# Optimization experiments

Measured on AMD Instinct MI355X. Metric: run time of the kernel, lower is better.

## Reference

```python
import jax, jax.numpy as jnp
import numpy as np

N, E = 50000, 1_000_000
IN_F, OUT_F = 128, 64
NEG_SLOPE = 0.2


def setup_inputs() -> dict:
    key = jax.random.key(0)
    k1, k2, k3, k4, k5 = jax.random.split(key, 5)
    x = jax.random.normal(k1, (N, IN_F), dtype=jnp.float32)
    edge_index = jax.random.randint(k2, (2, E), 0, N, dtype=jnp.int64)
    # xavier_uniform with gain=1.414 (as in the torch init)
    gain = 1.414
    bW = gain * np.sqrt(6.0 / (IN_F + OUT_F))
    W = jax.random.uniform(k3, (IN_F, OUT_F), jnp.float32, -bW, bW)
    ba = gain * np.sqrt(6.0 / (OUT_F + 1))
    a_src = jax.random.uniform(k4, (OUT_F, 1), jnp.float32, -ba, ba)
    a_dst = jax.random.uniform(k5, (OUT_F, 1), jnp.float32, -ba, ba)
    return {"x": x, "edge_index": edge_index, "W": W, "a_src": a_src, "a_dst": a_dst}


def reference(x, edge_index, W, a_src, a_dst):
    n = x.shape[0]
    Wh = x @ W                                  # [N, F_out]
    src = edge_index[0]
    dst = edge_index[1]
    # per-edge attention logits: (Wh[src] . a_src) + (Wh[dst] . a_dst)
    s_src = Wh @ a_src[:, 0]                    # [N]
    s_dst = Wh @ a_dst[:, 0]                    # [N]
    e = jax.nn.leaky_relu(s_src[src] + s_dst[dst], negative_slope=NEG_SLOPE)  # [E]
    e = jnp.exp(e - jnp.max(e))                 # global-max stabilized exp (matches torch code)
    denom = jax.ops.segment_sum(e, dst, num_segments=n) + 1e-16  # [N]
    alpha = e / denom[dst]                      # [E]  (dropout p=0 -> identity)
    out = jax.ops.segment_sum(Wh[src] * alpha[:, None], dst, num_segments=n)  # [N, F_out]
    return jax.nn.elu(out)
```

## Files before the change

kernel.cpp:

```cpp
#include <hip/hip_runtime.h>
#include <hip/hip_bf16.h>
#include <math.h>

#define NN 50000
#define NE 1000000
#define FIN 128
#define FOUT 64
#define NEG 0.2f

#define NB   2048
#define DPB  25
#define NBUSED 2000
#define TS   4096
#define NT   245
#define RCAP 1024
#define TILE_BLKS 245
#define GEMM_BLKS 391

using short8  = __attribute__((ext_vector_type(8))) short;
using floatx4 = __attribute__((ext_vector_type(4))) float;
using floatx2 = __attribute__((ext_vector_type(2))) float;

static __device__ __forceinline__ short f2bf(float f) {
    __hip_bfloat16 h = __float2bfloat16(f);
    return *(short*)&h;
}

__global__ __launch_bounds__(512) void k_front(
    const float* __restrict__ x, const float* __restrict__ W,
    const float* __restrict__ a_src, const float* __restrict__ a_dst,
    const int* __restrict__ ei,
    __hip_bfloat16* __restrict__ Whb, float* __restrict__ s_src,
    float* __restrict__ s_dst,
    unsigned* __restrict__ bdata, int* __restrict__ gofs)
{
    __shared__ int shmem_i[8192];
    __shared__ int wsum[8];

    const int tid  = threadIdx.x;
    const int lane = tid & 63;
    const int wv   = tid >> 6;

    if (blockIdx.x >= TILE_BLKS) {
        short* Wbt = (short*)shmem_i;

        #pragma unroll
        for (int rep = 0; rep < 16; ++rep) {
            const int e = rep * 512 + tid;
            const int k = e >> 6, n = e & 63;
            Wbt[n * 128 + (((k >> 3) ^ (n & 15)) << 3) + (k & 7)] = f2bf(W[e]);
        }
        __syncthreads();

        const int col  = lane & 15;
        const int quad = lane >> 4;
        const int strip = (blockIdx.x - TILE_BLKS) * 8 + wv;
        if (strip >= NN / 16) return;
        const int row0 = strip * 16;

        short8 bfr[4][4];
        #pragma unroll
        for (int kk = 0; kk < 4; ++kk) {
            #pragma unroll
            for (int nt = 0; nt < 4; ++nt) {
                const int n = nt * 16 + col;
                bfr[kk][nt] = *(const short8*)(
                    Wbt + n * 128 + ((((kk << 2) + quad) ^ (n & 15)) << 3));
            }
        }

        floatx4 acc[4] = {{0.f,0.f,0.f,0.f},{0.f,0.f,0.f,0.f},
                          {0.f,0.f,0.f,0.f},{0.f,0.f,0.f,0.f}};

        const float* xrow = x + (size_t)(row0 + col) * FIN + quad * 8;
        #pragma unroll
        for (int kk = 0; kk < 4; ++kk) {
            const floatx4 u0 = __builtin_nontemporal_load(
                (const floatx4*)(xrow + kk * 32));
            const floatx4 u1 = __builtin_nontemporal_load(
                (const floatx4*)(xrow + kk * 32 + 4));
            short8 af;
            af[0] = f2bf(u0[0]); af[1] = f2bf(u0[1]);
            af[2] = f2bf(u0[2]); af[3] = f2bf(u0[3]);
            af[4] = f2bf(u1[0]); af[5] = f2bf(u1[1]);
            af[6] = f2bf(u1[2]); af[7] = f2bf(u1[3]);
            #pragma unroll
            for (int nt = 0; nt < 4; ++nt)
                acc[nt] = __builtin_amdgcn_mfma_f32_16x16x32_bf16(
                    af, bfr[kk][nt], acc[nt], 0, 0, 0);
        }

        const float av0 = a_src[col], av1 = a_src[16 + col];
        const float av2 = a_src[32 + col], av3 = a_src[48 + col];
        const float bv0 = a_dst[col], bv1 = a_dst[16 + col];
        const float bv2 = a_dst[32 + col], bv3 = a_dst[48 + col];

        float ps[4], pd[4];
        #pragma unroll
        for (int reg = 0; reg < 4; ++reg) {
            ps[reg] = acc[0][reg] * av0 + acc[1][reg] * av1
                    + acc[2][reg] * av2 + acc[3][reg] * av3;
            pd[reg] = acc[0][reg] * bv0 + acc[1][reg] * bv1
                    + acc[2][reg] * bv2 + acc[3][reg] * bv3;
        }

        #pragma unroll
        for (int nt = 0; nt < 4; ++nt)
            #pragma unroll
            for (int reg = 0; reg < 4; ++reg)
                Whb[(size_t)(row0 + quad * 4 + reg) * FOUT + nt * 16 + col] =
                    __float2bfloat16(acc[nt][reg]);

        #pragma unroll
        for (int off = 1; off < 16; off <<= 1) {
            #pragma unroll
            for (int reg = 0; reg < 4; ++reg) {
                ps[reg] += __shfl_xor(ps[reg], off);
                pd[reg] += __shfl_xor(pd[reg], off);
            }
        }
        if (col == 0) {
            #pragma unroll
            for (int reg = 0; reg < 4; ++reg) {
                s_src[row0 + quad * 4 + reg] = ps[reg];
                s_dst[row0 + quad * 4 + reg] = pd[reg];
            }
        }
        return;
    }

    int* cnt = shmem_i;
    int* cur = shmem_i + NB;
    unsigned* srt = (unsigned*)(shmem_i + 2 * NB);

    const int tile = blockIdx.x;
    const int base = tile * TS;
    const int tcnt = (NE - base < TS) ? (NE - base) : TS;

    for (int i = tid; i < NB; i += 512) cnt[i] = 0;
    __syncthreads();

    unsigned pk[8];
    #pragma unroll
    for (int j = 0; j < 8; ++j) {
        const int i = j * 512 + tid;
        if (i < tcnt) {
            const int e = base + i;
            const unsigned s = (unsigned)__builtin_nontemporal_load(ei + e);
            const unsigned d = (unsigned)__builtin_nontemporal_load(ei + NE + e);
            pk[j] = (s << 16) | d;
            atomicAdd(&cnt[d / DPB], 1);
        } else pk[j] = 0xFFFFFFFFu;
    }
    __syncthreads();

    {
        const int i0 = tid * 4;
        const int v0 = cnt[i0], v1 = cnt[i0 + 1];
        const int v2 = cnt[i0 + 2], v3 = cnt[i0 + 3];
        const int s = v0 + v1 + v2 + v3;
        int inc = s;
        #pragma unroll
        for (int off = 1; off < 64; off <<= 1) {
            const int t = __shfl_up(inc, off);
            if (lane >= off) inc += t;
        }
        if (lane == 63) wsum[wv] = inc;
        __syncthreads();
        int wb = 0;
        #pragma unroll
        for (int w = 0; w < 7; ++w) if (w < wv) wb += wsum[w];
        const int excl = wb + inc - s;
        cur[i0]     = excl;
        cur[i0 + 1] = excl + v0;
        cur[i0 + 2] = excl + v0 + v1;
        cur[i0 + 3] = excl + v0 + v1 + v2;
        *(int4*)(gofs + (size_t)tile * NB + i0) =
            make_int4(excl, excl + v0, excl + v0 + v1, excl + v0 + v1 + v2);
    }
    __syncthreads();

    #pragma unroll
    for (int j = 0; j < 8; ++j) {
        if (pk[j] != 0xFFFFFFFFu) {
            const int b = (int)(pk[j] & 0xffffu) / DPB;
            const int pos = atomicAdd(&cur[b], 1);
            srt[pos] = pk[j];
        }
    }
    __syncthreads();

    for (int i = tid; i < tcnt; i += 512)
        bdata[base + i] = srt[i];
}

__global__ __launch_bounds__(256) void k_sortgather(
    const int* __restrict__ gofs, const unsigned* __restrict__ bdata,
    const float* __restrict__ s_src, const float* __restrict__ s_dst,
    const __hip_bfloat16* __restrict__ Whb, float* __restrict__ out)
{
    __shared__ unsigned raw[RCAP];
    __shared__ uint2 pes[RCAP];
    __shared__ float sdl[32];
    __shared__ int cnt[32];
    __shared__ int ofs2[33];
    __shared__ int cur[32];
    __shared__ int wsum[4];

    const int b = (blockIdx.x & 7) * 250 + (blockIdx.x >> 3);
    const int tid = threadIdx.x;
    const int lane = tid & 63;
    const int wv = tid >> 6;
    const int d0 = b * DPB;

    if (tid < 32) {
        cnt[tid] = 0;
        sdl[tid] = (tid < DPB) ? s_dst[d0 + tid] : 0.f;
    }

    int c = 0, o = 0;
    if (tid < NT) {
        const int* gp = gofs + (size_t)tid * NB + b;
        o = gp[0];
        c = gp[1] - o;
    }
    int inc = c;
    #pragma unroll
    for (int off = 1; off < 64; off <<= 1) {
        const int t = __shfl_up(inc, off);
        if (lane >= off) inc += t;
    }
    if (lane == 63) wsum[wv] = inc;
    __syncthreads();
    int wb = 0;
    #pragma unroll
    for (int w = 0; w < 3; ++w) if (w < wv) wb += wsum[w];
    const int segbase = wb + inc - c;
    int tot = wsum[0] + wsum[1] + wsum[2] + wsum[3];
    if (tot > RCAP) tot = RCAP;

    {
        const unsigned* bsrc = bdata + (size_t)tid * TS + o;
        int lim = RCAP - segbase; if (lim > c) lim = c; if (lim < 0) lim = 0;
        for (int k = 0; k < lim; ++k)
            raw[segbase + k] = bsrc[k];
    }
    __syncthreads();

    for (int i = tid; i < tot; i += 256)
        atomicAdd(&cnt[(int)(raw[i] & 0xffffu) - d0], 1);
    __syncthreads();

    if (tid < 32) {
        const int cc = (tid < DPB) ? cnt[tid] : 0;
        int in2 = cc;
        #pragma unroll
        for (int off = 1; off < 32; off <<= 1) {
            const int t = __shfl_up(in2, off);
            if (tid >= off) in2 += t;
        }
        ofs2[tid + 1] = in2;
        if (tid == 0) ofs2[0] = 0;
        cur[tid] = in2 - cc;
    }
    __syncthreads();

    for (int i = tid; i < tot; i += 256) {
        const unsigned p = raw[i];
        const int j = (int)(p & 0xffffu) - d0;
        const int pos = atomicAdd(&cur[j], 1);
        float v = s_src[p >> 16] + sdl[j];
        v = (v > 0.f) ? v : NEG * v;
        pes[pos] = make_uint2((p & 0xffff0000u) >> 9,
                              __float_as_uint(__expf(v)));
    }
    __syncthreads();

    const int q4 = lane >> 4;
    const int l4 = lane & 15;
    const char* wbase = (const char*)Whb + (l4 << 3);
    for (int j = wv; j < DPB; j += 4) {
        const int d = d0 + j;
        const int beg = ofs2[j];
        const int end = ofs2[j + 1];
        float a0 = 0.f, a1 = 0.f, a2 = 0.f, a3 = 0.f, dacc = 0.f;
        int i = beg;
        #define GBODY(idx)                                                 \
            {                                                              \
                const uint2 q = pes[idx];                                  \
                const float ev = __uint_as_float(q.y);                     \
                const uint2 u = *(const uint2*)(wbase + q.x);              \
                a0 = fmaf(ev, __uint_as_float(u.x << 16), a0);             \
                a1 = fmaf(ev, __uint_as_float(u.x & 0xffff0000u), a1);     \
                a2 = fmaf(ev, __uint_as_float(u.y << 16), a2);             \
                a3 = fmaf(ev, __uint_as_float(u.y & 0xffff0000u), a3);     \
                dacc += ev;                                                \
            }
        for (; i + 8 <= end; i += 8) {
            GBODY(i + q4)
            GBODY(i + 4 + q4)
        }
        for (; i + 4 <= end; i += 4)
            GBODY(i + q4)
        if (i < end && q4 < end - i)
            GBODY(i + q4)
        #undef GBODY
        a0 += __shfl_xor(a0, 16); a1 += __shfl_xor(a1, 16);
        a2 += __shfl_xor(a2, 16); a3 += __shfl_xor(a3, 16);
        dacc += __shfl_xor(dacc, 16);
        a0 += __shfl_xor(a0, 32); a1 += __shfl_xor(a1, 32);
        a2 += __shfl_xor(a2, 32); a3 += __shfl_xor(a3, 32);
        dacc += __shfl_xor(dacc, 32);
        if (lane < 16) {
            const float rd = 1.f / (dacc + 1e-16f);
            float r0 = a0 * rd, r1 = a1 * rd;
            float r2 = a2 * rd, r3 = a3 * rd;
            r0 = (r0 > 0.f) ? r0 : expm1f(r0);
            r1 = (r1 > 0.f) ? r1 : expm1f(r1);
            r2 = (r2 > 0.f) ? r2 : expm1f(r2);
            r3 = (r3 > 0.f) ? r3 : expm1f(r3);
            floatx4 rr; rr[0] = r0; rr[1] = r1; rr[2] = r2; rr[3] = r3;
            __builtin_nontemporal_store(
                rr, (floatx4*)(out + (size_t)d * FOUT) + l4);
        }
    }
}

extern "C" void kernel_launch(void* const* d_in, const int* in_sizes, int n_in,
                              void* d_out, int out_size, void* d_ws, size_t ws_size,
                              hipStream_t stream)
{
    const float* x     = (const float*)d_in[0];
    const int*   ei    = (const int*)d_in[1];
    const float* W     = (const float*)d_in[2];
    const float* a_src = (const float*)d_in[3];
    const float* a_dst = (const float*)d_in[4];
    float* out = (float*)d_out;

    float* ws    = (float*)d_ws;
    __hip_bfloat16* Whb = (__hip_bfloat16*)ws;
    float* s_src = ws + (size_t)NN * FOUT / 2;
    float* s_dst = s_src + NN;
    int*   gofs  = (int*)(s_dst + NN);
    unsigned* bdata = (unsigned*)(gofs + (size_t)NT * NB);

    k_front<<<TILE_BLKS + GEMM_BLKS, 512, 0, stream>>>(
        x, W, a_src, a_dst, ei, Whb, s_src, s_dst, bdata, gofs);
    k_sortgather<<<NBUSED, 256, 0, stream>>>(gofs, bdata, s_src, s_dst,
                                             Whb, out);
}
```

Baseline: 118.1 us.

## Loop GEMM strips per block, vectorize edge loads, fuse count pass, unroll gather

The GEMM blocks now process four 16-row strips each, cutting the block count so the W tile staging and B-fragment loads are amortized across more work. The edge-tile front end loads src/dst indices as 4-wide vectors, with each thread handling eight contiguous edges instead of strided ones. The per-bucket histogram is folded into the raw copy loop, which removes one pass and one barrier. The gather loop gains a 16-edge unrolled body for more memory-level parallelism. In exchange there are fewer GEMM blocks in flight, and the vector loads assume 16-byte alignment of the tile base.

```diff
diff --git a/kernel.cpp b/kernel.cpp
--- a/kernel.cpp
+++ b/kernel.cpp
@@ -15,11 +15,13 @@
 #define NT   245
 #define RCAP 1024
 #define TILE_BLKS 245
-#define GEMM_BLKS 391
+#define SITER 4
+#define GEMM_BLKS 98
 
 using short8  = __attribute__((ext_vector_type(8))) short;
 using floatx4 = __attribute__((ext_vector_type(4))) float;
 using floatx2 = __attribute__((ext_vector_type(2))) float;
+using intx4   = __attribute__((ext_vector_type(4))) int;
 
 static __device__ __forceinline__ short f2bf(float f) {
     __hip_bfloat16 h = __float2bfloat16(f);
@@ -54,9 +56,6 @@
 
         const int col  = lane & 15;
         const int quad = lane >> 4;
-        const int strip = (blockIdx.x - TILE_BLKS) * 8 + wv;
-        if (strip >= NN / 16) return;
-        const int row0 = strip * 16;
 
         short8 bfr[4][4];
         #pragma unroll
@@ -68,62 +67,68 @@
                     Wbt + n * 128 + ((((kk << 2) + quad) ^ (n & 15)) << 3));
             }
         }
-
-        floatx4 acc[4] = {{0.f,0.f,0.f,0.f},{0.f,0.f,0.f,0.f},
-                          {0.f,0.f,0.f,0.f},{0.f,0.f,0.f,0.f}};
-
-        const float* xrow = x + (size_t)(row0 + col) * FIN + quad * 8;
-        #pragma unroll
-        for (int kk = 0; kk < 4; ++kk) {
-            const floatx4 u0 = __builtin_nontemporal_load(
-                (const floatx4*)(xrow + kk * 32));
-            const floatx4 u1 = __builtin_nontemporal_load(
-                (const floatx4*)(xrow + kk * 32 + 4));
-            short8 af;
-            af[0] = f2bf(u0[0]); af[1] = f2bf(u0[1]);
-            af[2] = f2bf(u0[2]); af[3] = f2bf(u0[3]);
-            af[4] = f2bf(u1[0]); af[5] = f2bf(u1[1]);
-            af[6] = f2bf(u1[2]); af[7] = f2bf(u1[3]);
-            #pragma unroll
-            for (int nt = 0; nt < 4; ++nt)
-                acc[nt] = __builtin_amdgcn_mfma_f32_16x16x32_bf16(
-                    af, bfr[kk][nt], acc[nt], 0, 0, 0);
-        }
-
         const float av0 = a_src[col], av1 = a_src[16 + col];
         const float av2 = a_src[32 + col], av3 = a_src[48 + col];
         const float bv0 = a_dst[col], bv1 = a_dst[16 + col];
         const float bv2 = a_dst[32 + col], bv3 = a_dst[48 + col];
 
-        float ps[4], pd[4];
-        #pragma unroll
-        for (int reg = 0; reg < 4; ++reg) {
-            ps[reg] = acc[0][reg] * av0 + acc[1][reg] * av1
-                    + acc[2][reg] * av2 + acc[3][reg] * av3;
-            pd[reg] = acc[0][reg] * bv0 + acc[1][reg] * bv1
-                    + acc[2][reg] * bv2 + acc[3][reg] * bv3;
-        }
-
-        #pragma unroll
-        for (int nt = 0; nt < 4; ++nt)
-            #pragma unroll
-            for (int reg = 0; reg < 4; ++reg)
-                Whb[(size_t)(row0 + quad * 4 + reg) * FOUT + nt * 16 + col] =
-                    __float2bfloat16(acc[nt][reg]);
-
-        #pragma unroll
-        for (int off = 1; off < 16; off <<= 1) {
+        const int sbase = (blockIdx.x - TILE_BLKS) * (8 * SITER);
+        for (int it = 0; it < SITER; ++it) {
+            const int strip = sbase + it * 8 + wv;
+            if (strip >= NN / 16) break;
+            const int row0 = strip * 16;
+
+            floatx4 acc[4] = {{0.f,0.f,0.f,0.f},{0.f,0.f,0.f,0.f},
+                              {0.f,0.f,0.f,0.f},{0.f,0.f,0.f,0.f}};
+
+            const float* xrow = x + (size_t)(row0 + col) * FIN + quad * 8;
+            #pragma unroll
+            for (int kk = 0; kk < 4; ++kk) {
+                const floatx4 u0 = __builtin_nontemporal_load(
+                    (const floatx4*)(xrow + kk * 32));
+                const floatx4 u1 = __builtin_nontemporal_load(
+                    (const floatx4*)(xrow + kk * 32 + 4));
+                short8 af;
+                af[0] = f2bf(u0[0]); af[1] = f2bf(u0[1]);
+                af[2] = f2bf(u0[2]); af[3] = f2bf(u0[3]);
+                af[4] = f2bf(u1[0]); af[5] = f2bf(u1[1]);
+                af[6] = f2bf(u1[2]); af[7] = f2bf(u1[3]);
+                #pragma unroll
+                for (int nt = 0; nt < 4; ++nt)
+                    acc[nt] = __builtin_amdgcn_mfma_f32_16x16x32_bf16(
+                        af, bfr[kk][nt], acc[nt], 0, 0, 0);
+            }
+
+            float ps[4], pd[4];
             #pragma unroll
             for (int reg = 0; reg < 4; ++reg) {
-                ps[reg] += __shfl_xor(ps[reg], off);
-                pd[reg] += __shfl_xor(pd[reg], off);
-            }
-        }
-        if (col == 0) {
-            #pragma unroll
-            for (int reg = 0; reg < 4; ++reg) {
-                s_src[row0 + quad * 4 + reg] = ps[reg];
-                s_dst[row0 + quad * 4 + reg] = pd[reg];
+                ps[reg] = acc[0][reg] * av0 + acc[1][reg] * av1
+                        + acc[2][reg] * av2 + acc[3][reg] * av3;
+                pd[reg] = acc[0][reg] * bv0 + acc[1][reg] * bv1
+                        + acc[2][reg] * bv2 + acc[3][reg] * bv3;
+            }
+
+            #pragma unroll
+            for (int nt = 0; nt < 4; ++nt)
+                #pragma unroll
+                for (int reg = 0; reg < 4; ++reg)
+                    Whb[(size_t)(row0 + quad * 4 + reg) * FOUT + nt * 16 + col] =
+                        __float2bfloat16(acc[nt][reg]);
+
+            #pragma unroll
+            for (int off = 1; off < 16; off <<= 1) {
+                #pragma unroll
+                for (int reg = 0; reg < 4; ++reg) {
+                    ps[reg] += __shfl_xor(ps[reg], off);
+                    pd[reg] += __shfl_xor(pd[reg], off);
+                }
+            }
+            if (col == 0) {
+                #pragma unroll
+                for (int reg = 0; reg < 4; ++reg) {
+                    s_src[row0 + quad * 4 + reg] = ps[reg];
+                    s_dst[row0 + quad * 4 + reg] = pd[reg];
+                }
             }
         }
         return;
@@ -141,16 +146,29 @@
     __syncthreads();
 
     unsigned pk[8];
-    #pragma unroll
-    for (int j = 0; j < 8; ++j) {
-        const int i = j * 512 + tid;
-        if (i < tcnt) {
-            const int e = base + i;
-            const unsigned s = (unsigned)__builtin_nontemporal_load(ei + e);
-            const unsigned d = (unsigned)__builtin_nontemporal_load(ei + NE + e);
-            pk[j] = (s << 16) | d;
-            atomicAdd(&cnt[d / DPB], 1);
-        } else pk[j] = 0xFFFFFFFFu;
+    {
+        const int i0e = tid * 8;
+        if (i0e < tcnt) {
+            const int e = base + i0e;
+            const intx4 s0 = __builtin_nontemporal_load((const intx4*)(ei + e));
+            const intx4 s1 = __builtin_nontemporal_load((const intx4*)(ei + e + 4));
+            const intx4 d0 = __builtin_nontemporal_load((const intx4*)(ei + NE + e));
+            const intx4 d1 = __builtin_nontemporal_load((const intx4*)(ei + NE + e + 4));
+            pk[0] = ((unsigned)s0[0] << 16) | (unsigned)d0[0];
+            pk[1] = ((unsigned)s0[1] << 16) | (unsigned)d0[1];
+            pk[2] = ((unsigned)s0[2] << 16) | (unsigned)d0[2];
+            pk[3] = ((unsigned)s0[3] << 16) | (unsigned)d0[3];
+            pk[4] = ((unsigned)s1[0] << 16) | (unsigned)d1[0];
+            pk[5] = ((unsigned)s1[1] << 16) | (unsigned)d1[1];
+            pk[6] = ((unsigned)s1[2] << 16) | (unsigned)d1[2];
+            pk[7] = ((unsigned)s1[3] << 16) | (unsigned)d1[3];
+            #pragma unroll
+            for (int j = 0; j < 8; ++j)
+                atomicAdd(&cnt[(int)(pk[j] & 0xffffu) / DPB], 1);
+        } else {
+            #pragma unroll
+            for (int j = 0; j < 8; ++j) pk[j] = 0xFFFFFFFFu;
+        }
     }
     __syncthreads();
 
@@ -242,13 +260,12 @@
     {
         const unsigned* bsrc = bdata + (size_t)tid * TS + o;
         int lim = RCAP - segbase; if (lim > c) lim = c; if (lim < 0) lim = 0;
-        for (int k = 0; k < lim; ++k)
-            raw[segbase + k] = bsrc[k];
-    }
-    __syncthreads();
-
-    for (int i = tid; i < tot; i += 256)
-        atomicAdd(&cnt[(int)(raw[i] & 0xffffu) - d0], 1);
+        for (int k = 0; k < lim; ++k) {
+            const unsigned v = bsrc[k];
+            raw[segbase + k] = v;
+            atomicAdd(&cnt[(int)(v & 0xffffu) - d0], 1);
+        }
+    }
     __syncthreads();
 
     if (tid < 32) {
@@ -296,6 +313,12 @@
                 a3 = fmaf(ev, __uint_as_float(u.y & 0xffff0000u), a3);     \
                 dacc += ev;                                                \
             }
+        for (; i + 16 <= end; i += 16) {
+            GBODY(i + q4)
+            GBODY(i + 4 + q4)
+            GBODY(i + 8 + q4)
+            GBODY(i + 12 + q4)
+        }
         for (; i + 8 <= end; i += 8) {
             GBODY(i + q4)
             GBODY(i + 4 + q4)
```

Result: slower. 127.2 us (+7.7%).
